# Kernel optimization log

Measured on AMD Instinct MI355X. Metric: run time of the kernel, lower is better.

## Reference

```python
import jax, jax.numpy as jnp
import numpy as np
from jax import lax

TOP, LEFT, BOTTOM, RIGHT = 0, 1, 2, 3
IOU_THR = 0.5
CLASS_OFFSET = 1e5  # separates classes so cross-class IoU == 0 (class-aware NMS trick)

B, N, C = 8, 2000, 81


def setup_inputs() -> dict:
    key = jax.random.key(0)
    k1, k2, k3, k4, k5 = jax.random.split(key, 5)
    # nms_reg: plausible (top, left, bottom, right) boxes with positive extent
    tl = jax.random.uniform(k1, (B, N, 2), dtype=jnp.float32) * 500.0
    wh = jax.random.uniform(k2, (B, N, 2), dtype=jnp.float32) * 100.0 + 1.0
    nms_reg = jnp.concatenate([tl, tl + wh], axis=2)  # [B,N,4] tlbr
    nms_cls = jax.random.normal(k3, (B, N, 2), dtype=jnp.float32)
    rcnn_reg = jax.random.normal(k4, (B, N, 4), dtype=jnp.float32)  # small refinements
    rcnn_cls = jax.random.normal(k5, (B, N, C), dtype=jnp.float32)
    return {"nms_reg": nms_reg, "nms_cls": nms_cls, "rcnn_reg": rcnn_reg,
            "rcnn_cls": rcnn_cls, "reduction": 16}


def _pairwise_iou(boxes):
    # boxes: [N,4] in (top,left,bottom,right)
    t, l, b, r = boxes[:, 0], boxes[:, 1], boxes[:, 2], boxes[:, 3]
    area = (b - t) * (r - l)
    it = jnp.maximum(t[:, None], t[None, :])
    il = jnp.maximum(l[:, None], l[None, :])
    ib = jnp.minimum(b[:, None], b[None, :])
    ir = jnp.minimum(r[:, None], r[None, :])
    inter = jnp.clip(ib - it, 0.0) * jnp.clip(ir - il, 0.0)
    union = area[:, None] + area[None, :] - inter
    return inter / jnp.maximum(union, 1e-9)


def _nms_image(boxes, probs):
    # boxes: [N,4], probs: [N,C]. Greedy per-class NMS (class-aware via offsets).
    cls_arg = jnp.argmax(probs, axis=1)                                # [N]
    scores = jnp.take_along_axis(probs, cls_arg[:, None], axis=1)[:, 0]  # prob of predicted class
    valid = cls_arg != 0                                               # drop background
    off_boxes = boxes + (cls_arg.astype(boxes.dtype) * CLASS_OFFSET)[:, None]
    order = jnp.argsort(-jnp.where(valid, scores, -jnp.inf))
    sb = off_boxes[order]
    sv = valid[order]
    iou = _pairwise_iou(sb)                                            # [N,N]
    n = boxes.shape[0]
    idx = jnp.arange(n)

    def body(i, keep):
        sup = keep[i] & (iou[i] > IOU_THR) & (idx > i)
        return keep & ~sup

    keep_sorted = lax.fori_loop(0, n, body, sv)
    # back to original order
    return jnp.zeros(n, dtype=bool).at[order].set(keep_sorted)


def reference(nms_reg, nms_cls, rcnn_reg, rcnn_cls, reduction):
    red = jnp.asarray(reduction, dtype=nms_reg.dtype)
    nms_reg_rounded = jnp.concatenate(
        [jnp.floor(nms_reg[:, :, 0:2] * red), jnp.ceil(nms_reg[:, :, 2:4] * red)],
        axis=2) / red
    rcnn_reg_adj = rcnn_reg + nms_reg_rounded                          # [B,N,4]
    probs = jax.nn.softmax(rcnn_cls, axis=2)                           # [B,N,C]
    keep = jax.vmap(_nms_image)(rcnn_reg_adj, probs)                   # [B,N] bool
    # fixed-shape equivalent of the ragged per-image lists: zero-out suppressed rows
    reg_out = jnp.where(keep[:, :, None], rcnn_reg_adj, 0.0)
    cls_out = jnp.where(keep[:, :, None], probs, 0.0)
    return nms_reg, nms_cls, rcnn_reg_adj, probs, reg_out, cls_out, keep
```

## Files before the change

### kernel.cpp

```cpp
#include <hip/hip_runtime.h>
#include <math.h>

constexpr int B_ = 8;
constexpr int N_ = 2000;
constexpr int C_ = 81;
constexpr int BN = B_ * N_;

constexpr int O0 = 0;
constexpr int O1 = 64000;
constexpr int O2 = 96000;
constexpr int O3 = 160000;
constexpr int O4 = 1456000;
constexpr int O5 = 1520000;
constexpr int O6 = 2816000;

__global__ __launch_bounds__(256) void prep_kernel(
    const float* __restrict__ nms_reg, const float* __restrict__ nms_cls,
    const float* __restrict__ rcnn_reg, const float* __restrict__ rcnn_cls,
    const int* __restrict__ reduction,
    float* __restrict__ out, float* __restrict__ scores, int* __restrict__ clsArg)
{
    int gid  = blockIdx.x * blockDim.x + threadIdx.x;
    int wave = gid >> 6;
    int lane = threadIdx.x & 63;
    if (wave >= BN) return;

    if (gid < 16000) {
        ((float4*)(out + O0))[gid] = ((const float4*)nms_reg)[gid];
    } else if (gid < 24000) {
        int g = gid - 16000;
        ((float4*)(out + O1))[g] = ((const float4*)nms_cls)[g];
    }

    const float* lg = rcnn_cls + (size_t)wave * C_;
    float x0 = lg[lane];
    float x1 = (lane < C_ - 64) ? lg[lane + 64] : -INFINITY;

    float m = fmaxf(x0, x1);
    for (int off = 32; off; off >>= 1) m = fmaxf(m, __shfl_xor(m, off, 64));

    float e0 = expf(x0 - m);
    float e1 = (lane < C_ - 64) ? expf(x1 - m) : 0.0f;
    float s = e0 + e1;
    for (int off = 32; off; off >>= 1) s += __shfl_xor(s, off, 64);

    float p0 = e0 / s;
    float p1 = e1 / s;

    float* probs = out + O3 + (size_t)wave * C_;
    probs[lane] = p0;
    if (lane < C_ - 64) probs[lane + 64] = p1;

    float v = p0; int idx = lane;
    if (lane < C_ - 64 && p1 > p0) { v = p1; idx = lane + 64; }
    for (int off = 32; off; off >>= 1) {
        float ov = __shfl_xor(v, off, 64);
        int   oi = __shfl_xor(idx, off, 64);
        if (ov > v || (ov == v && oi < idx)) { v = ov; idx = oi; }
    }

    if (lane < 4) {
        float red = (float)reduction[0];
        float t = nms_reg[(size_t)wave * 4 + lane] * red;
        float r = (lane < 2) ? floorf(t) : ceilf(t);
        out[O2 + (size_t)wave * 4 + lane] =
            rcnn_reg[(size_t)wave * 4 + lane] + r / red;
    }

    if (idx == 0) {
        float* co = out + O5 + (size_t)wave * C_;
        co[lane] = 0.0f;
        if (lane < C_ - 64) co[lane + 64] = 0.0f;
        if (lane < 4) out[O4 + (size_t)wave * 4 + lane] = 0.0f;
    }

    if (lane == 0) {
        scores[wave] = v;
        clsArg[wave] = idx;
        out[O6 + wave] = 0.0f;
    }
}

__global__ __launch_bounds__(256) void classnms_kernel(
    const int* __restrict__ clsArg, const float* __restrict__ scores,
    float* __restrict__ out)
{
    __shared__ int   list[N_];
    __shared__ float sc[N_];
    __shared__ int   srt[N_];
    __shared__ int   cnt;

    int b = blockIdx.x / (C_ - 1);
    int c = blockIdx.x % (C_ - 1) + 1;
    int tid  = threadIdx.x;
    int lane = tid & 63;
    int w    = tid >> 6;

    if (tid == 0) cnt = 0;
    __syncthreads();

    const int STRIP = N_ / 4;
    for (int it = 0; it < (STRIP + 63) / 64; it++) {
        int n = w * STRIP + it * 64 + lane;
        bool m = false;
        float sv = 0.0f;
        if (n < (w + 1) * STRIP) {
            m  = (clsArg[b * N_ + n] == c);
            sv = scores[b * N_ + n];
        }
        unsigned long long bal = __ballot(m);
        int nset = __popcll(bal);
        int base = 0;
        if (lane == 0 && nset) base = atomicAdd(&cnt, nset);
        base = __shfl(base, 0, 64);
        if (m) {
            int pos = base + __popcll(bal & ((1ull << lane) - 1ull));
            list[pos] = n;
            sc[pos]   = sv;
        }
    }
    __syncthreads();
    int k = cnt;
    if (k == 0) return;

    for (int t = tid; t < k; t += 256) {
        int   my  = list[t];
        float mys = sc[t];
        int rank = 0;
        for (int j = 0; j < k; j++) {
            float os = sc[j];
            rank += (os > mys) || (os == mys && list[j] < my);
        }
        srt[rank] = my;
    }
    __syncthreads();

    const float* boxes4 = out + O2;
    if (w == 0) {
        float off = (float)c * 100000.0f;

        float t0 = 0, l0 = 0, bb0 = 0, r0 = 0, a0 = 0;
        if (lane < k) {
            const float* p = boxes4 + (size_t)(b * N_ + srt[lane]) * 4;
            t0 = p[0] + off; l0 = p[1] + off; bb0 = p[2] + off; r0 = p[3] + off;
            a0 = (bb0 - t0) * (r0 - l0);
        }

        int nch = (k + 63) >> 6;
        unsigned int keepm = 0;
        for (int ch = 0; ch < nch; ch++) if (ch * 64 + lane < k) keepm |= (1u << ch);

        for (int i = 0; i < k; i++) {
            int ich = i >> 6, il = i & 63;
            unsigned int wi = __shfl(keepm, il, 64);
            if (!((wi >> ich) & 1)) continue;

            float ti, li, bi, ri, ai;
            if (ich == 0) {
                ti = __shfl(t0, il, 64); li = __shfl(l0, il, 64);
                bi = __shfl(bb0, il, 64); ri = __shfl(r0, il, 64);
                ai = __shfl(a0, il, 64);
            } else {
                const float* p = boxes4 + (size_t)(b * N_ + srt[i]) * 4;
                ti = p[0] + off; li = p[1] + off; bi = p[2] + off; ri = p[3] + off;
                ai = (bi - ti) * (ri - li);
            }

            for (int ch = ich; ch < nch; ch++) {
                int j = ch * 64 + lane;
                if (j <= i || j >= k) continue;
                if (!((keepm >> ch) & 1)) continue;
                float tj, lj, bj, rj, aj;
                if (ch == 0) { tj = t0; lj = l0; bj = bb0; rj = r0; aj = a0; }
                else {
                    const float* p = boxes4 + (size_t)(b * N_ + srt[j]) * 4;
                    tj = p[0] + off; lj = p[1] + off; bj = p[2] + off; rj = p[3] + off;
                    aj = (bj - tj) * (rj - lj);
                }
                float it2 = fmaxf(ti, tj), il2 = fmaxf(li, lj);
                float ib = fminf(bi, bj), ir = fminf(ri, rj);
                float inter = fmaxf(ib - it2, 0.0f) * fmaxf(ir - il2, 0.0f);
                float uni = ai + aj - inter;
                if (inter / fmaxf(uni, 1e-9f) > 0.5f) keepm &= ~(1u << ch);
            }
        }

        for (int ch = 0; ch < nch; ch++) {
            int j = ch * 64 + lane;
            if (j < k) list[j] = (keepm >> ch) & 1;
        }
    }
    __syncthreads();

    for (int p = tid; p < k; p += 256) {
        int g = b * N_ + srt[p];
        int kept = list[p];
        out[O6 + g] = kept ? 1.0f : 0.0f;
        float4 adj = ((const float4*)(out + O2))[g];
        ((float4*)(out + O4))[g] = kept ? adj : float4{0.f, 0.f, 0.f, 0.f};
    }
    for (int idx = tid; idx < k * C_; idx += 256) {
        int p = idx / C_, e = idx - p * C_;
        int g = b * N_ + srt[p];
        out[O5 + (size_t)g * C_ + e] =
            list[p] ? out[O3 + (size_t)g * C_ + e] : 0.0f;
    }
}

extern "C" void kernel_launch(void* const* d_in, const int* in_sizes, int n_in,
                              void* d_out, int out_size, void* d_ws, size_t ws_size,
                              hipStream_t stream)
{
    const float* nms_reg   = (const float*)d_in[0];
    const float* nms_cls   = (const float*)d_in[1];
    const float* rcnn_reg  = (const float*)d_in[2];
    const float* rcnn_cls  = (const float*)d_in[3];
    const int*   reduction = (const int*)d_in[4];
    float* out = (float*)d_out;

    float* scores = (float*)d_ws;
    int*   clsArg = (int*)d_ws + 16000;

    prep_kernel<<<(BN * 64) / 256, 256, 0, stream>>>(
        nms_reg, nms_cls, rcnn_reg, rcnn_cls, reduction, out, scores, clsArg);
    classnms_kernel<<<B_ * (C_ - 1), 256, 0, stream>>>(clsArg, scores, out);
}
```

Measured before the change: 101.2 us.

## Parallelize small-class NMS via suppression bitmasks and prewrite kept outputs

For classes with at most 64 boxes, each thread computes a suppression bitmask against all earlier boxes in parallel from shared memory, and one thread then resolves the greedy keep mask serially. This replaces the single-wave serial loop with shuffles. The prep kernel now writes cls_out and reg_out as if every box were kept, so the NMS kernel only writes zeros for suppressed boxes instead of copying probabilities. Class and score are packed into a single int2 for the gather. The cost is extra writes in prep, plus a serial resolve over 64 bits per block done by one thread.

Measured after the change: 90.88 us. 10.2% less time.

```diff
diff --git a/kernel.cpp b/kernel.cpp
--- a/kernel.cpp
+++ b/kernel.cpp
@@ -18,7 +18,7 @@
     const float* __restrict__ nms_reg, const float* __restrict__ nms_cls,
     const float* __restrict__ rcnn_reg, const float* __restrict__ rcnn_cls,
     const int* __restrict__ reduction,
-    float* __restrict__ out, float* __restrict__ scores, int* __restrict__ clsArg)
+    float* __restrict__ out, int2* __restrict__ packed)
 {
     int gid  = blockIdx.x * blockDim.x + threadIdx.x;
     int wave = gid >> 6;
@@ -46,10 +46,6 @@
 
     float p0 = e0 / s;
     float p1 = e1 / s;
-
-    float* probs = out + O3 + (size_t)wave * C_;
-    probs[lane] = p0;
-    if (lane < C_ - 64) probs[lane + 64] = p1;
 
     float v = p0; int idx = lane;
     if (lane < C_ - 64 && p1 > p0) { v = p1; idx = lane + 64; }
@@ -58,37 +54,40 @@
         int   oi = __shfl_xor(idx, off, 64);
         if (ov > v || (ov == v && oi < idx)) { v = ov; idx = oi; }
     }
+    bool valid = (idx != 0);
+
+    float* probs = out + O3 + (size_t)wave * C_;
+    float* co    = out + O5 + (size_t)wave * C_;
+    probs[lane] = p0;
+    co[lane]    = valid ? p0 : 0.0f;
+    if (lane < C_ - 64) {
+        probs[lane + 64] = p1;
+        co[lane + 64]    = valid ? p1 : 0.0f;
+    }
 
     if (lane < 4) {
         float red = (float)reduction[0];
         float t = nms_reg[(size_t)wave * 4 + lane] * red;
         float r = (lane < 2) ? floorf(t) : ceilf(t);
-        out[O2 + (size_t)wave * 4 + lane] =
-            rcnn_reg[(size_t)wave * 4 + lane] + r / red;
-    }
-
-    if (idx == 0) {
-        float* co = out + O5 + (size_t)wave * C_;
-        co[lane] = 0.0f;
-        if (lane < C_ - 64) co[lane + 64] = 0.0f;
-        if (lane < 4) out[O4 + (size_t)wave * 4 + lane] = 0.0f;
+        float adj = rcnn_reg[(size_t)wave * 4 + lane] + r / red;
+        out[O2 + (size_t)wave * 4 + lane] = adj;
+        out[O4 + (size_t)wave * 4 + lane] = valid ? adj : 0.0f;
     }
 
     if (lane == 0) {
-        scores[wave] = v;
-        clsArg[wave] = idx;
+        packed[wave] = make_int2(idx, __float_as_int(v));
         out[O6 + wave] = 0.0f;
     }
 }
 
 __global__ __launch_bounds__(256) void classnms_kernel(
-    const int* __restrict__ clsArg, const float* __restrict__ scores,
-    float* __restrict__ out)
+    const int2* __restrict__ packed, float* __restrict__ out)
 {
     __shared__ int   list[N_];
     __shared__ float sc[N_];
     __shared__ int   srt[N_];
     __shared__ int   cnt;
+    __shared__ unsigned long long keep_sh;
 
     int b = blockIdx.x / (C_ - 1);
     int c = blockIdx.x % (C_ - 1) + 1;
@@ -100,13 +99,15 @@
     __syncthreads();
 
     const int STRIP = N_ / 4;
+    #pragma unroll
     for (int it = 0; it < (STRIP + 63) / 64; it++) {
         int n = w * STRIP + it * 64 + lane;
         bool m = false;
         float sv = 0.0f;
         if (n < (w + 1) * STRIP) {
-            m  = (clsArg[b * N_ + n] == c);
-            sv = scores[b * N_ + n];
+            int2 pc = packed[b * N_ + n];
+            m  = (pc.x == c);
+            sv = __int_as_float(pc.y);
         }
         unsigned long long bal = __ballot(m);
         int nset = __popcll(bal);
@@ -136,74 +137,116 @@
     __syncthreads();
 
     const float* boxes4 = out + O2;
-    if (w == 0) {
-        float off = (float)c * 100000.0f;
-
-        float t0 = 0, l0 = 0, bb0 = 0, r0 = 0, a0 = 0;
-        if (lane < k) {
-            const float* p = boxes4 + (size_t)(b * N_ + srt[lane]) * 4;
-            t0 = p[0] + off; l0 = p[1] + off; bb0 = p[2] + off; r0 = p[3] + off;
-            a0 = (bb0 - t0) * (r0 - l0);
-        }
-
-        int nch = (k + 63) >> 6;
-        unsigned int keepm = 0;
-        for (int ch = 0; ch < nch; ch++) if (ch * 64 + lane < k) keepm |= (1u << ch);
-
-        for (int i = 0; i < k; i++) {
-            int ich = i >> 6, il = i & 63;
-            unsigned int wi = __shfl(keepm, il, 64);
-            if (!((wi >> ich) & 1)) continue;
-
-            float ti, li, bi, ri, ai;
-            if (ich == 0) {
-                ti = __shfl(t0, il, 64); li = __shfl(l0, il, 64);
-                bi = __shfl(bb0, il, 64); ri = __shfl(r0, il, 64);
-                ai = __shfl(a0, il, 64);
-            } else {
-                const float* p = boxes4 + (size_t)(b * N_ + srt[i]) * 4;
-                ti = p[0] + off; li = p[1] + off; bi = p[2] + off; ri = p[3] + off;
-                ai = (bi - ti) * (ri - li);
-            }
-
-            for (int ch = ich; ch < nch; ch++) {
-                int j = ch * 64 + lane;
-                if (j <= i || j >= k) continue;
-                if (!((keepm >> ch) & 1)) continue;
-                float tj, lj, bj, rj, aj;
-                if (ch == 0) { tj = t0; lj = l0; bj = bb0; rj = r0; aj = a0; }
-                else {
-                    const float* p = boxes4 + (size_t)(b * N_ + srt[j]) * 4;
-                    tj = p[0] + off; lj = p[1] + off; bj = p[2] + off; rj = p[3] + off;
-                    aj = (bj - tj) * (rj - lj);
-                }
+    float off = (float)c * 100000.0f;
+
+    if (k <= 64) {
+        float* bt  = sc;
+        float* bl  = sc + 64;
+        float* bb2 = sc + 128;
+        float* br  = sc + 192;
+        float* ba  = sc + 256;
+        unsigned long long* supm = (unsigned long long*)(sc + 320);
+
+        if (tid < k) {
+            float4 p = ((const float4*)boxes4)[b * N_ + srt[tid]];
+            float t = p.x + off, l = p.y + off, bo = p.z + off, r = p.w + off;
+            bt[tid]  = t;  bl[tid] = l;  bb2[tid] = bo;  br[tid] = r;
+            ba[tid]  = (bo - t) * (r - l);
+        }
+        __syncthreads();
+
+        if (tid < k) {
+            float tj = bt[tid], lj = bl[tid], bj = bb2[tid], rj = br[tid], aj = ba[tid];
+            unsigned long long msk = 0ull;
+            for (int i = 0; i < k; i++) {
+                float ti = bt[i], li = bl[i], bi = bb2[i], ri = br[i], ai = ba[i];
                 float it2 = fmaxf(ti, tj), il2 = fmaxf(li, lj);
                 float ib = fminf(bi, bj), ir = fminf(ri, rj);
                 float inter = fmaxf(ib - it2, 0.0f) * fmaxf(ir - il2, 0.0f);
                 float uni = ai + aj - inter;
-                if (inter / fmaxf(uni, 1e-9f) > 0.5f) keepm &= ~(1u << ch);
-            }
-        }
-
-        for (int ch = 0; ch < nch; ch++) {
-            int j = ch * 64 + lane;
-            if (j < k) list[j] = (keepm >> ch) & 1;
+                bool sup = (inter / fmaxf(uni, 1e-9f) > 0.5f) && (i < tid);
+                msk |= sup ? (1ull << i) : 0ull;
+            }
+            supm[tid] = msk;
+        }
+        __syncthreads();
+
+        if (tid == 0) {
+            unsigned long long keep = (k == 64) ? ~0ull : ((1ull << k) - 1ull);
+            for (int j = 1; j < k; j++)
+                if (supm[j] & keep) keep &= ~(1ull << j);
+            keep_sh = keep;
+        }
+        __syncthreads();
+        unsigned long long keep = keep_sh;
+        for (int p = tid; p < k; p += 256) list[p] = (int)((keep >> p) & 1ull);
+    } else {
+        if (w == 0) {
+            float t0 = 0, l0 = 0, bb0 = 0, r0 = 0, a0 = 0;
+            if (lane < k) {
+                const float* p = boxes4 + (size_t)(b * N_ + srt[lane]) * 4;
+                t0 = p[0] + off; l0 = p[1] + off; bb0 = p[2] + off; r0 = p[3] + off;
+                a0 = (bb0 - t0) * (r0 - l0);
+            }
+
+            int nch = (k + 63) >> 6;
+            unsigned int keepm = 0;
+            for (int ch = 0; ch < nch; ch++) if (ch * 64 + lane < k) keepm |= (1u << ch);
+
+            for (int i = 0; i < k; i++) {
+                int ich = i >> 6, il = i & 63;
+                unsigned int wi = __shfl(keepm, il, 64);
+                if (!((wi >> ich) & 1)) continue;
+
+                float ti, li, bi, ri, ai;
+                if (ich == 0) {
+                    ti = __shfl(t0, il, 64); li = __shfl(l0, il, 64);
+                    bi = __shfl(bb0, il, 64); ri = __shfl(r0, il, 64);
+                    ai = __shfl(a0, il, 64);
+                } else {
+                    const float* p = boxes4 + (size_t)(b * N_ + srt[i]) * 4;
+                    ti = p[0] + off; li = p[1] + off; bi = p[2] + off; ri = p[3] + off;
+                    ai = (bi - ti) * (ri - li);
+                }
+
+                for (int ch = ich; ch < nch; ch++) {
+                    int j = ch * 64 + lane;
+                    if (j <= i || j >= k) continue;
+                    if (!((keepm >> ch) & 1)) continue;
+                    float tj, lj, bj, rj, aj;
+                    if (ch == 0) { tj = t0; lj = l0; bj = bb0; rj = r0; aj = a0; }
+                    else {
+                        const float* p = boxes4 + (size_t)(b * N_ + srt[j]) * 4;
+                        tj = p[0] + off; lj = p[1] + off; bj = p[2] + off; rj = p[3] + off;
+                        aj = (bj - tj) * (rj - lj);
+                    }
+                    float it2 = fmaxf(ti, tj), il2 = fmaxf(li, lj);
+                    float ib = fminf(bi, bj), ir = fminf(ri, rj);
+                    float inter = fmaxf(ib - it2, 0.0f) * fmaxf(ir - il2, 0.0f);
+                    float uni = ai + aj - inter;
+                    if (inter / fmaxf(uni, 1e-9f) > 0.5f) keepm &= ~(1u << ch);
+                }
+            }
+
+            for (int ch = 0; ch < nch; ch++) {
+                int j = ch * 64 + lane;
+                if (j < k) list[j] = (keepm >> ch) & 1;
+            }
         }
     }
     __syncthreads();
 
     for (int p = tid; p < k; p += 256) {
         int g = b * N_ + srt[p];
-        int kept = list[p];
-        out[O6 + g] = kept ? 1.0f : 0.0f;
-        float4 adj = ((const float4*)(out + O2))[g];
-        ((float4*)(out + O4))[g] = kept ? adj : float4{0.f, 0.f, 0.f, 0.f};
+        if (list[p]) out[O6 + g] = 1.0f;
+        else         ((float4*)(out + O4))[g] = float4{0.f, 0.f, 0.f, 0.f};
     }
     for (int idx = tid; idx < k * C_; idx += 256) {
         int p = idx / C_, e = idx - p * C_;
-        int g = b * N_ + srt[p];
-        out[O5 + (size_t)g * C_ + e] =
-            list[p] ? out[O3 + (size_t)g * C_ + e] : 0.0f;
+        if (!list[p]) {
+            int g = b * N_ + srt[p];
+            out[O5 + (size_t)g * C_ + e] = 0.0f;
+        }
     }
 }
 
@@ -218,10 +261,9 @@
     const int*   reduction = (const int*)d_in[4];
     float* out = (float*)d_out;
 
-    float* scores = (float*)d_ws;
-    int*   clsArg = (int*)d_ws + 16000;
+    int2* packed = (int2*)d_ws;
 
     prep_kernel<<<(BN * 64) / 256, 256, 0, stream>>>(
-        nms_reg, nms_cls, rcnn_reg, rcnn_cls, reduction, out, scores, clsArg);
-    classnms_kernel<<<B_ * (C_ - 1), 256, 0, stream>>>(clsArg, scores, out);
+        nms_reg, nms_cls, rcnn_reg, rcnn_cls, reduction, out, packed);
+    classnms_kernel<<<B_ * (C_ - 1), 256, 0, stream>>>(packed, out);
 }
```
